# Kernel tuning notes

Measured on AMD Instinct MI355X. Metric: run time of the kernel, lower is better.

The kernel has to match this reference:

```python
import jax, jax.numpy as jnp
import numpy as np

N, E, D_IN, D_OUT = 50000, 800000, 96, 256
BN_EPS = 1e-3  # Keras BatchNormalization default epsilon


def setup_inputs() -> dict:
    key = jax.random.key(0)
    ks = jax.random.split(key, 8)
    return {
        "x": jax.random.normal(ks[0], (N, D_IN), dtype=jnp.float32),
        "adj_src": jax.random.randint(ks[1], (E,), 0, N, dtype=jnp.int32),
        "adj_dst": jax.random.randint(ks[2], (E,), 0, N, dtype=jnp.int32),
        "adj_vals": jax.random.uniform(ks[3], (E,), dtype=jnp.float32),
        "eps": jax.random.normal(ks[4], (1,), dtype=jnp.float32) * 0.05,
        "W0": jax.random.normal(ks[5], (D_IN, D_OUT), dtype=jnp.float32) * 0.05,
        "W1": jax.random.normal(ks[6], (D_OUT, D_OUT), dtype=jnp.float32) * 0.05,
        "gamma": jnp.ones((D_OUT,), dtype=jnp.float32),
        "beta": jnp.zeros((D_OUT,), dtype=jnp.float32),
        "bn_mean": jnp.zeros((D_OUT,), dtype=jnp.float32),
        "bn_var": jnp.ones((D_OUT,), dtype=jnp.float32),
    }


def reference(x, adj_src, adj_dst, adj_vals, eps, W0, W1, gamma, beta, bn_mean, bn_var):
    n = x.shape[0]
    # Sparse adjacency SpMM: out[d] = sum_{e: dst(e)=d} vals[e] * x[src(e)]
    msgs = adj_vals[:, None] * x[adj_src]              # [E, D_IN]
    agg = jax.ops.segment_sum(msgs, adj_dst, num_segments=n)  # [N, D_IN]
    h = agg + eps * x                                   # eps residual (GIN)
    # MLP layer 0: matmul -> BN (inference) -> ReLU (dropout identity at eval)
    h = h @ W0                                           # [N, D_OUT]
    h = (h - bn_mean) * jax.lax.rsqrt(bn_var + BN_EPS) * gamma + beta
    h = jax.nn.relu(h)
    # Final matmul
    return h @ W1                                        # [N, D_OUT]
```

## Files before the change

### kernel.cpp

```cpp
#include <hip/hip_runtime.h>

#define D_IN   96
#define D_OUT  256
#define BN_EPS 1e-3f
#define TROWS  32
#define CAP    64
#define N_PAD  50048
#define RS1    104
#define RS2    264

typedef __attribute__((ext_vector_type(8))) short  short8;
typedef __attribute__((ext_vector_type(4))) float  floatx4;

__device__ __forceinline__ unsigned short f2bf(float f) {
    unsigned int u = __float_as_uint(f);
    unsigned int r = u + 0x7FFFu + ((u >> 16) & 1u);
    return (unsigned short)(r >> 16);
}
__device__ __forceinline__ float bfbits(unsigned short u) {
    return __uint_as_float(((unsigned int)u) << 16);
}

template<bool BF16X>
__device__ __forceinline__ void load12(const float* __restrict__ x,
                                       const unsigned short* __restrict__ xbf,
                                       int rowid, int cg, float* o)
{
    if (BF16X) {
        const unsigned short* r = xbf + (size_t)rowid * D_IN + cg * 12;
        ushort4 a = *(const ushort4*)(r);
        ushort4 b = *(const ushort4*)(r + 4);
        ushort4 c = *(const ushort4*)(r + 8);
        o[0] = bfbits(a.x); o[1] = bfbits(a.y); o[2]  = bfbits(a.z); o[3]  = bfbits(a.w);
        o[4] = bfbits(b.x); o[5] = bfbits(b.y); o[6]  = bfbits(b.z); o[7]  = bfbits(b.w);
        o[8] = bfbits(c.x); o[9] = bfbits(c.y); o[10] = bfbits(c.z); o[11] = bfbits(c.w);
    } else {
        const float* r = x + (size_t)rowid * D_IN + cg * 12;
        float4 A = *(const float4*)(r);
        float4 B = *(const float4*)(r + 4);
        float4 C = *(const float4*)(r + 8);
        o[0] = A.x; o[1] = A.y; o[2]  = A.z; o[3]  = A.w;
        o[4] = B.x; o[5] = B.y; o[6]  = B.z; o[7]  = B.w;
        o[8] = C.x; o[9] = C.y; o[10] = C.z; o[11] = C.w;
    }
}

__global__ __launch_bounds__(256) void prep(
    const int* __restrict__ src, const int* __restrict__ dst,
    const float* __restrict__ vals, const float* __restrict__ x,
    const float* __restrict__ W0, const float* __restrict__ W1,
    int* __restrict__ cursor, int* __restrict__ bucket,
    unsigned short* __restrict__ xbf,
    unsigned short* __restrict__ W0p, unsigned short* __restrict__ W1p,
    int E4, int n, int nscat, int nxc)
{
    const int b = blockIdx.x, tid = threadIdx.x;
    if (b < nscat) {
        int t = b * 256 + tid;
        if (t < E4) {
            int4   d4 = ((const int4*)dst)[t];
            int4   s4 = ((const int4*)src)[t];
            float4 v4 = ((const float4*)vals)[t];
#define PUT(dd, ss, vv)                                                    \
            {  unsigned int u = __float_as_uint(vv);                       \
               unsigned int vhi = (u + 0x7FFFu + ((u >> 16) & 1u)) & 0xFFFF0000u; \
               int pos = atomicAdd(&cursor[dd], 1);                        \
               if (pos < CAP) bucket[((dd) << 6) + pos] = (int)(vhi | (unsigned int)(ss)); }
            PUT(d4.x, s4.x, v4.x)
            PUT(d4.y, s4.y, v4.y)
            PUT(d4.z, s4.z, v4.z)
            PUT(d4.w, s4.w, v4.w)
#undef PUT
        }
    } else if (b < nscat + nxc) {
        int t = (b - nscat) * 256 + tid;
        if (t * 4 < n * D_IN) {
            float4 v = *(const float4*)(x + (size_t)t * 4);
            ushort4 o;
            o.x = f2bf(v.x); o.y = f2bf(v.y); o.z = f2bf(v.z); o.w = f2bf(v.w);
            *(ushort4*)(xbf + (size_t)t * 4) = o;
        }
    } else {
        int o = (b - nscat - nxc) * 256 + tid;
        const int n0 = 3 * 256 * 32;
        const int n1 = 8 * 256 * 32;
        if (o < n0) {
            int kk = o & 31, nn = (o >> 5) & 255, kb = o >> 13;
            W0p[o] = f2bf(W0[(size_t)(kb * 32 + kk) * 256 + nn]);
        } else if (o < n0 + n1) {
            int o2 = o - n0;
            int kk = o2 & 31, nn = (o2 >> 5) & 255, kb = o2 >> 13;
            W1p[o2] = f2bf(W1[(size_t)(kb * 32 + kk) * 256 + nn]);
        }
    }
}

template<bool BF16X>
__global__ __launch_bounds__(256) void gin_fused(
    const float* __restrict__ x, const unsigned short* __restrict__ xbf,
    const int* __restrict__ deg, const int* __restrict__ bucket,
    const float* __restrict__ epsp,
    const unsigned short* __restrict__ W0p, const unsigned short* __restrict__ W1p,
    const float* __restrict__ gamma, const float* __restrict__ beta,
    const float* __restrict__ bn_mean, const float* __restrict__ bn_var,
    float* __restrict__ out, int n)
{
    __shared__ __align__(16) unsigned short Abuf[TROWS][RS1];
    __shared__ __align__(16) unsigned short Hbuf[TROWS][RS2];
    __shared__ float bn_scale[D_OUT];
    __shared__ float bn_shift[D_OUT];

    const int tid = threadIdx.x;
    const int rowbase = blockIdx.x * TROWS;
    const float epsv = *epsp;

    {
        float sc = gamma[tid] * rsqrtf(bn_var[tid] + BN_EPS);
        bn_scale[tid] = sc;
        bn_shift[tid] = fmaf(-bn_mean[tid], sc, beta[tid]);
    }

    {
        const int w  = tid >> 6;
        const int es = (tid & 63) >> 3;
        const int cg = tid & 7;

        for (int rr = 0; rr < 8; ++rr) {
            const int rl  = w * 8 + rr;
            const int row = rowbase + rl;
            float accp[12];
#pragma unroll
            for (int q = 0; q < 12; ++q) accp[q] = 0.f;

            if (row < n) {
                const int dg = min(deg[row], CAP);
                const int* ep = bucket + (row << 6);
                int e = es;
                for (; e + 8 < dg; e += 16) {
                    int p0 = ep[e], p1 = ep[e + 8];
                    float r0[12], r1[12];
                    load12<BF16X>(x, xbf, p0 & 0xFFFF, cg, r0);
                    load12<BF16X>(x, xbf, p1 & 0xFFFF, cg, r1);
                    float v0 = __uint_as_float((unsigned int)p0 & 0xFFFF0000u);
                    float v1 = __uint_as_float((unsigned int)p1 & 0xFFFF0000u);
#pragma unroll
                    for (int q = 0; q < 12; ++q) {
                        accp[q] = fmaf(v0, r0[q], accp[q]);
                        accp[q] = fmaf(v1, r1[q], accp[q]);
                    }
                }
                if (e < dg) {
                    int p0 = ep[e];
                    float r0[12];
                    load12<BF16X>(x, xbf, p0 & 0xFFFF, cg, r0);
                    float v0 = __uint_as_float((unsigned int)p0 & 0xFFFF0000u);
#pragma unroll
                    for (int q = 0; q < 12; ++q)
                        accp[q] = fmaf(v0, r0[q], accp[q]);
                }
            }

#pragma unroll
            for (int q = 0; q < 12; ++q) {
                accp[q] += __shfl_xor(accp[q], 8, 64);
                accp[q] += __shfl_xor(accp[q], 16, 64);
                accp[q] += __shfl_xor(accp[q], 32, 64);
            }

            if (es == 0) {
                if (row < n) {
                    float rx[12];
                    load12<BF16X>(x, xbf, row, cg, rx);
#pragma unroll
                    for (int q = 0; q < 12; ++q)
                        accp[q] = fmaf(epsv, rx[q], accp[q]);
                }
#pragma unroll
                for (int q = 0; q < 6; ++q) {
                    unsigned int lo = f2bf(accp[2 * q]);
                    unsigned int hi = f2bf(accp[2 * q + 1]);
                    *(unsigned int*)&Abuf[rl][cg * 12 + 2 * q] = lo | (hi << 16);
                }
            }
        }
    }
    __syncthreads();

    const int lane = tid & 63;
    const int wid  = tid >> 6;
    const int quad = lane >> 4;
    const int nl   = lane & 15;

    floatx4 acc1[2][4];
#pragma unroll
    for (int mt = 0; mt < 2; ++mt)
#pragma unroll
        for (int nt = 0; nt < 4; ++nt)
            acc1[mt][nt] = (floatx4){0.f, 0.f, 0.f, 0.f};

#pragma unroll
    for (int kb = 0; kb < 3; ++kb) {
        short8 af0 = *(const short8*)&Abuf[nl     ][kb * 32 + quad * 8];
        short8 af1 = *(const short8*)&Abuf[16 + nl][kb * 32 + quad * 8];
#pragma unroll
        for (int nt = 0; nt < 4; ++nt) {
            const unsigned short* bp =
                W0p + ((size_t)(kb * 256 + wid * 64 + nt * 16 + nl)) * 32 + quad * 8;
            short8 bf = *(const short8*)bp;
            acc1[0][nt] = __builtin_amdgcn_mfma_f32_16x16x32_bf16(af0, bf, acc1[0][nt], 0, 0, 0);
            acc1[1][nt] = __builtin_amdgcn_mfma_f32_16x16x32_bf16(af1, bf, acc1[1][nt], 0, 0, 0);
        }
    }

#pragma unroll
    for (int mt = 0; mt < 2; ++mt)
#pragma unroll
        for (int nt = 0; nt < 4; ++nt) {
            int ncol = wid * 64 + nt * 16 + nl;
            float sc = bn_scale[ncol], sh = bn_shift[ncol];
#pragma unroll
            for (int r = 0; r < 4; ++r) {
                float h = fmaxf(0.f, fmaf(acc1[mt][nt][r], sc, sh));
                Hbuf[mt * 16 + quad * 4 + r][ncol] = f2bf(h);
            }
        }
    __syncthreads();

    floatx4 acc2[2][4];
#pragma unroll
    for (int mt = 0; mt < 2; ++mt)
#pragma unroll
        for (int nt = 0; nt < 4; ++nt)
            acc2[mt][nt] = (floatx4){0.f, 0.f, 0.f, 0.f};

#pragma unroll
    for (int kb = 0; kb < 8; ++kb) {
        short8 af0 = *(const short8*)&Hbuf[nl     ][kb * 32 + quad * 8];
        short8 af1 = *(const short8*)&Hbuf[16 + nl][kb * 32 + quad * 8];
#pragma unroll
        for (int nt = 0; nt < 4; ++nt) {
            const unsigned short* bp =
                W1p + ((size_t)(kb * 256 + wid * 64 + nt * 16 + nl)) * 32 + quad * 8;
            short8 bf = *(const short8*)bp;
            acc2[0][nt] = __builtin_amdgcn_mfma_f32_16x16x32_bf16(af0, bf, acc2[0][nt], 0, 0, 0);
            acc2[1][nt] = __builtin_amdgcn_mfma_f32_16x16x32_bf16(af1, bf, acc2[1][nt], 0, 0, 0);
        }
    }

#pragma unroll
    for (int mt = 0; mt < 2; ++mt)
#pragma unroll
        for (int nt = 0; nt < 4; ++nt) {
            int ncol = wid * 64 + nt * 16 + nl;
#pragma unroll
            for (int r = 0; r < 4; ++r) {
                int m = rowbase + mt * 16 + quad * 4 + r;
                if (m < n) out[(size_t)m * D_OUT + ncol] = acc2[mt][nt][r];
            }
        }
}

extern "C" void kernel_launch(void* const* d_in, const int* in_sizes, int n_in,
                              void* d_out, int out_size, void* d_ws, size_t ws_size,
                              hipStream_t stream) {
    const float* x       = (const float*)d_in[0];
    const int*   src     = (const int*)  d_in[1];
    const int*   dst     = (const int*)  d_in[2];
    const float* vals    = (const float*)d_in[3];
    const float* epsp    = (const float*)d_in[4];
    const float* W0      = (const float*)d_in[5];
    const float* W1      = (const float*)d_in[6];
    const float* gamma   = (const float*)d_in[7];
    const float* beta    = (const float*)d_in[8];
    const float* bn_mean = (const float*)d_in[9];
    const float* bn_var  = (const float*)d_in[10];
    float* out = (float*)d_out;

    const int n = in_sizes[0] / D_IN;
    const int E = in_sizes[1];

    int* cursor = (int*)d_ws;
    int* bucket = cursor + N_PAD;
    unsigned short* W0p = (unsigned short*)(bucket + (size_t)n * CAP);
    unsigned short* W1p = W0p + 3 * 256 * 32;
    unsigned short* xbf = W1p + 8 * 256 * 32;

    const size_t base_need = (size_t)(N_PAD + (size_t)n * CAP) * 4
                           + (size_t)(3 + 8) * 256 * 32 * 2;
    const bool use_bf16x = ws_size >= base_need + (size_t)n * D_IN * 2;

    hipMemsetAsync(cursor, 0, (size_t)n * sizeof(int), stream);

    const int E4    = E / 4;
    const int nscat = (E4 + 255) / 256;
    const int nxc   = use_bf16x ? (n * D_IN / 4 + 255) / 256 : 0;
    const int nwc   = ((3 + 8) * 256 * 32 + 255) / 256;
    prep<<<nscat + nxc + nwc, 256, 0, stream>>>(
        src, dst, vals, x, W0, W1, cursor, bucket, xbf, W0p, W1p, E4, n, nscat, nxc);

    const int gblocks = (n + TROWS - 1) / TROWS;
    if (use_bf16x)
        gin_fused<true><<<gblocks, 256, 0, stream>>>(
            x, xbf, cursor, bucket, epsp, W0p, W1p,
            gamma, beta, bn_mean, bn_var, out, n);
    else
        gin_fused<false><<<gblocks, 256, 0, stream>>>(
            x, xbf, cursor, bucket, epsp, W0p, W1p,
            gamma, beta, bn_mean, bn_var, out, n);
}
```

Baseline: 229.4 us.

## Make each wave own 16 rows end-to-end and split atomic cursors by edge parity

The fused kernel is restructured so that each wavefront processes its own 16 rows through gather, both MFMA matmuls and the store, which removes the block-wide __syncthreads barriers. In the gather, 4 lanes now cover one row with 24 features each, replacing the 8-way edge split and its shuffle reduction. The scatter builds two sub-buckets per destination, keyed by edge parity, to halve contention on each atomic counter. BN scale and shift are precomputed once in the prep kernel. The trade-off is that every wave now reads all of W0 and W1 on its own, the per-lane register footprint grows, and each sub-bucket is capped at 32 edges.

```diff
diff --git a/kernel.cpp b/kernel.cpp
--- a/kernel.cpp
+++ b/kernel.cpp
@@ -1,16 +1,17 @@
 #include <hip/hip_runtime.h>
 
-#define D_IN   96
-#define D_OUT  256
-#define BN_EPS 1e-3f
-#define TROWS  32
-#define CAP    64
-#define N_PAD  50048
-#define RS1    104
-#define RS2    264
-
-typedef __attribute__((ext_vector_type(8))) short  short8;
-typedef __attribute__((ext_vector_type(4))) float  floatx4;
+#define D_IN    96
+#define D_OUT   256
+#define BN_EPS  1e-3f
+#define CAP     64
+#define SUBCAP  32
+#define N_PAD   50048
+#define RS1     104
+#define RS2     264
+
+typedef __attribute__((ext_vector_type(8))) short          short8;
+typedef __attribute__((ext_vector_type(8))) unsigned short ushort8;
+typedef __attribute__((ext_vector_type(4))) float          floatx4;
 
 __device__ __forceinline__ unsigned short f2bf(float f) {
     unsigned int u = __float_as_uint(f);
@@ -22,26 +23,26 @@
 }
 
 template<bool BF16X>
-__device__ __forceinline__ void load12(const float* __restrict__ x,
+__device__ __forceinline__ void load24(const float* __restrict__ x,
                                        const unsigned short* __restrict__ xbf,
-                                       int rowid, int cg, float* o)
+                                       int rowid, int j, float* o)
 {
     if (BF16X) {
-        const unsigned short* r = xbf + (size_t)rowid * D_IN + cg * 12;
-        ushort4 a = *(const ushort4*)(r);
-        ushort4 b = *(const ushort4*)(r + 4);
-        ushort4 c = *(const ushort4*)(r + 8);
-        o[0] = bfbits(a.x); o[1] = bfbits(a.y); o[2]  = bfbits(a.z); o[3]  = bfbits(a.w);
-        o[4] = bfbits(b.x); o[5] = bfbits(b.y); o[6]  = bfbits(b.z); o[7]  = bfbits(b.w);
-        o[8] = bfbits(c.x); o[9] = bfbits(c.y); o[10] = bfbits(c.z); o[11] = bfbits(c.w);
+        const ushort8* p = (const ushort8*)(xbf + (size_t)rowid * D_IN + j * 24);
+        ushort8 a = p[0], b = p[1], c = p[2];
+#pragma unroll
+        for (int q = 0; q < 8; ++q) {
+            o[q]      = bfbits(a[q]);
+            o[8 + q]  = bfbits(b[q]);
+            o[16 + q] = bfbits(c[q]);
+        }
     } else {
-        const float* r = x + (size_t)rowid * D_IN + cg * 12;
-        float4 A = *(const float4*)(r);
-        float4 B = *(const float4*)(r + 4);
-        float4 C = *(const float4*)(r + 8);
-        o[0] = A.x; o[1] = A.y; o[2]  = A.z; o[3]  = A.w;
-        o[4] = B.x; o[5] = B.y; o[6]  = B.z; o[7]  = B.w;
-        o[8] = C.x; o[9] = C.y; o[10] = C.z; o[11] = C.w;
+        const float4* p = (const float4*)(x + (size_t)rowid * D_IN + j * 24);
+#pragma unroll
+        for (int q = 0; q < 6; ++q) {
+            float4 v = p[q];
+            o[4 * q] = v.x; o[4 * q + 1] = v.y; o[4 * q + 2] = v.z; o[4 * q + 3] = v.w;
+        }
     }
 }
 
@@ -49,28 +50,25 @@
     const int* __restrict__ src, const int* __restrict__ dst,
     const float* __restrict__ vals, const float* __restrict__ x,
     const float* __restrict__ W0, const float* __restrict__ W1,
+    const float* __restrict__ gamma, const float* __restrict__ beta,
+    const float* __restrict__ bn_mean, const float* __restrict__ bn_var,
     int* __restrict__ cursor, int* __restrict__ bucket,
     unsigned short* __restrict__ xbf,
     unsigned short* __restrict__ W0p, unsigned short* __restrict__ W1p,
-    int E4, int n, int nscat, int nxc)
+    float* __restrict__ bnsc, float* __restrict__ bnsh,
+    int E, int n, int nscat, int nxc)
 {
     const int b = blockIdx.x, tid = threadIdx.x;
     if (b < nscat) {
         int t = b * 256 + tid;
-        if (t < E4) {
-            int4   d4 = ((const int4*)dst)[t];
-            int4   s4 = ((const int4*)src)[t];
-            float4 v4 = ((const float4*)vals)[t];
-#define PUT(dd, ss, vv)                                                    \
-            {  unsigned int u = __float_as_uint(vv);                       \
-               unsigned int vhi = (u + 0x7FFFu + ((u >> 16) & 1u)) & 0xFFFF0000u; \
-               int pos = atomicAdd(&cursor[dd], 1);                        \
-               if (pos < CAP) bucket[((dd) << 6) + pos] = (int)(vhi | (unsigned int)(ss)); }
-            PUT(d4.x, s4.x, v4.x)
-            PUT(d4.y, s4.y, v4.y)
-            PUT(d4.z, s4.z, v4.z)
-            PUT(d4.w, s4.w, v4.w)
-#undef PUT
+        if (t < E) {
+            int d = dst[t];
+            unsigned int u = __float_as_uint(vals[t]);
+            unsigned int vhi = (u + 0x7FFFu + ((u >> 16) & 1u)) & 0xFFFF0000u;
+            int par = t & 1;
+            int pos = atomicAdd(&cursor[2 * d + par], 1);
+            if (pos < SUBCAP)
+                bucket[(d << 6) + par * SUBCAP + pos] = (int)(vhi | (unsigned int)src[t]);
         }
     } else if (b < nscat + nxc) {
         int t = (b - nscat) * 256 + tid;
@@ -91,6 +89,11 @@
             int o2 = o - n0;
             int kk = o2 & 31, nn = (o2 >> 5) & 255, kb = o2 >> 13;
             W1p[o2] = f2bf(W1[(size_t)(kb * 32 + kk) * 256 + nn]);
+        } else if (o < n0 + n1 + D_OUT) {
+            int col = o - n0 - n1;
+            float sc = gamma[col] * rsqrtf(bn_var[col] + BN_EPS);
+            bnsc[col] = sc;
+            bnsh[col] = fmaf(-bn_mean[col], sc, beta[col]);
         }
     }
 }
@@ -98,166 +101,135 @@
 template<bool BF16X>
 __global__ __launch_bounds__(256) void gin_fused(
     const float* __restrict__ x, const unsigned short* __restrict__ xbf,
-    const int* __restrict__ deg, const int* __restrict__ bucket,
+    const int* __restrict__ cursor, const int* __restrict__ bucket,
     const float* __restrict__ epsp,
     const unsigned short* __restrict__ W0p, const unsigned short* __restrict__ W1p,
-    const float* __restrict__ gamma, const float* __restrict__ beta,
-    const float* __restrict__ bn_mean, const float* __restrict__ bn_var,
+    const float* __restrict__ bnsc, const float* __restrict__ bnsh,
     float* __restrict__ out, int n)
 {
-    __shared__ __align__(16) unsigned short Abuf[TROWS][RS1];
-    __shared__ __align__(16) unsigned short Hbuf[TROWS][RS2];
-    __shared__ float bn_scale[D_OUT];
-    __shared__ float bn_shift[D_OUT];
-
-    const int tid = threadIdx.x;
-    const int rowbase = blockIdx.x * TROWS;
+    __shared__ __align__(16) unsigned short Abuf[4][16][RS1];
+    __shared__ __align__(16) unsigned short Hbuf[4][16][RS2];
+
+    const int tid  = threadIdx.x;
+    const int wv   = tid >> 6;
+    const int lane = tid & 63;
+    const int rowbase = blockIdx.x * 64 + wv * 16;
     const float epsv = *epsp;
 
     {
-        float sc = gamma[tid] * rsqrtf(bn_var[tid] + BN_EPS);
-        bn_scale[tid] = sc;
-        bn_shift[tid] = fmaf(-bn_mean[tid], sc, beta[tid]);
-    }
-
-    {
-        const int w  = tid >> 6;
-        const int es = (tid & 63) >> 3;
-        const int cg = tid & 7;
-
-        for (int rr = 0; rr < 8; ++rr) {
-            const int rl  = w * 8 + rr;
-            const int row = rowbase + rl;
-            float accp[12];
-#pragma unroll
-            for (int q = 0; q < 12; ++q) accp[q] = 0.f;
-
-            if (row < n) {
-                const int dg = min(deg[row], CAP);
-                const int* ep = bucket + (row << 6);
-                int e = es;
-                for (; e + 8 < dg; e += 16) {
-                    int p0 = ep[e], p1 = ep[e + 8];
-                    float r0[12], r1[12];
-                    load12<BF16X>(x, xbf, p0 & 0xFFFF, cg, r0);
-                    load12<BF16X>(x, xbf, p1 & 0xFFFF, cg, r1);
-                    float v0 = __uint_as_float((unsigned int)p0 & 0xFFFF0000u);
-                    float v1 = __uint_as_float((unsigned int)p1 & 0xFFFF0000u);
-#pragma unroll
-                    for (int q = 0; q < 12; ++q) {
-                        accp[q] = fmaf(v0, r0[q], accp[q]);
-                        accp[q] = fmaf(v1, r1[q], accp[q]);
-                    }
-                }
-                if (e < dg) {
-                    int p0 = ep[e];
-                    float r0[12];
-                    load12<BF16X>(x, xbf, p0 & 0xFFFF, cg, r0);
-                    float v0 = __uint_as_float((unsigned int)p0 & 0xFFFF0000u);
-#pragma unroll
-                    for (int q = 0; q < 12; ++q)
-                        accp[q] = fmaf(v0, r0[q], accp[q]);
+        const int rl = lane >> 2;
+        const int j  = lane & 3;
+        const int row = rowbase + rl;
+        float accp[24];
+#pragma unroll
+        for (int q = 0; q < 24; ++q) accp[q] = 0.f;
+
+        if (row < n) {
+            const int d0 = min(cursor[2 * row], SUBCAP);
+            const int d1 = min(cursor[2 * row + 1], SUBCAP);
+            const int cnt = d0 + d1;
+            const int* ep = bucket + ((size_t)row << 6);
+            int i = 0;
+            for (; i + 2 <= cnt; i += 2) {
+                int i0 = (i     < d0) ? i     : i     - d0 + SUBCAP;
+                int i1 = (i + 1 < d0) ? i + 1 : i + 1 - d0 + SUBCAP;
+                int p0 = ep[i0], p1 = ep[i1];
+                float r0[24], r1[24];
+                load24<BF16X>(x, xbf, p0 & 0xFFFF, j, r0);
+                load24<BF16X>(x, xbf, p1 & 0xFFFF, j, r1);
+                float v0 = __uint_as_float((unsigned int)p0 & 0xFFFF0000u);
+                float v1 = __uint_as_float((unsigned int)p1 & 0xFFFF0000u);
+#pragma unroll
+                for (int q = 0; q < 24; ++q) {
+                    accp[q] = fmaf(v0, r0[q], accp[q]);
+                    accp[q] = fmaf(v1, r1[q], accp[q]);
                 }
             }
-
-#pragma unroll
-            for (int q = 0; q < 12; ++q) {
-                accp[q] += __shfl_xor(accp[q], 8, 64);
-                accp[q] += __shfl_xor(accp[q], 16, 64);
-                accp[q] += __shfl_xor(accp[q], 32, 64);
+            if (i < cnt) {
+                int i0 = (i < d0) ? i : i - d0 + SUBCAP;
+                int p0 = ep[i0];
+                float r0[24];
+                load24<BF16X>(x, xbf, p0 & 0xFFFF, j, r0);
+                float v0 = __uint_as_float((unsigned int)p0 & 0xFFFF0000u);
+#pragma unroll
+                for (int q = 0; q < 24; ++q)
+                    accp[q] = fmaf(v0, r0[q], accp[q]);
             }
-
-            if (es == 0) {
-                if (row < n) {
-                    float rx[12];
-                    load12<BF16X>(x, xbf, row, cg, rx);
-#pragma unroll
-                    for (int q = 0; q < 12; ++q)
-                        accp[q] = fmaf(epsv, rx[q], accp[q]);
-                }
-#pragma unroll
-                for (int q = 0; q < 6; ++q) {
-                    unsigned int lo = f2bf(accp[2 * q]);
-                    unsigned int hi = f2bf(accp[2 * q + 1]);
-                    *(unsigned int*)&Abuf[rl][cg * 12 + 2 * q] = lo | (hi << 16);
-                }
-            }
-        }
-    }
-    __syncthreads();
-
-    const int lane = tid & 63;
-    const int wid  = tid >> 6;
+            float rx[24];
+            load24<BF16X>(x, xbf, row, j, rx);
+#pragma unroll
+            for (int q = 0; q < 24; ++q)
+                accp[q] = fmaf(epsv, rx[q], accp[q]);
+        }
+#pragma unroll
+        for (int g = 0; g < 3; ++g) {
+            short8 s;
+#pragma unroll
+            for (int q = 0; q < 8; ++q)
+                s[q] = (short)f2bf(accp[g * 8 + q]);
+            *(short8*)&Abuf[wv][rl][j * 24 + g * 8] = s;
+        }
+    }
+
     const int quad = lane >> 4;
     const int nl   = lane & 15;
 
-    floatx4 acc1[2][4];
-#pragma unroll
-    for (int mt = 0; mt < 2; ++mt)
-#pragma unroll
-        for (int nt = 0; nt < 4; ++nt)
-            acc1[mt][nt] = (floatx4){0.f, 0.f, 0.f, 0.f};
+    short8 af[3];
+#pragma unroll
+    for (int kb = 0; kb < 3; ++kb)
+        af[kb] = *(const short8*)&Abuf[wv][nl][kb * 32 + quad * 8];
+
+    floatx4 acc1[16];
+#pragma unroll
+    for (int nt = 0; nt < 16; ++nt)
+        acc1[nt] = (floatx4){0.f, 0.f, 0.f, 0.f};
 
 #pragma unroll
     for (int kb = 0; kb < 3; ++kb) {
-        short8 af0 = *(const short8*)&Abuf[nl     ][kb * 32 + quad * 8];
-        short8 af1 = *(const short8*)&Abuf[16 + nl][kb * 32 + quad * 8];
-#pragma unroll
-        for (int nt = 0; nt < 4; ++nt) {
-            const unsigned short* bp =
-                W0p + ((size_t)(kb * 256 + wid * 64 + nt * 16 + nl)) * 32 + quad * 8;
-            short8 bf = *(const short8*)bp;
-            acc1[0][nt] = __builtin_amdgcn_mfma_f32_16x16x32_bf16(af0, bf, acc1[0][nt], 0, 0, 0);
-            acc1[1][nt] = __builtin_amdgcn_mfma_f32_16x16x32_bf16(af1, bf, acc1[1][nt], 0, 0, 0);
-        }
-    }
-
-#pragma unroll
-    for (int mt = 0; mt < 2; ++mt)
-#pragma unroll
-        for (int nt = 0; nt < 4; ++nt) {
-            int ncol = wid * 64 + nt * 16 + nl;
-            float sc = bn_scale[ncol], sh = bn_shift[ncol];
-#pragma unroll
-            for (int r = 0; r < 4; ++r) {
-                float h = fmaxf(0.f, fmaf(acc1[mt][nt][r], sc, sh));
-                Hbuf[mt * 16 + quad * 4 + r][ncol] = f2bf(h);
-            }
-        }
-    __syncthreads();
-
-    floatx4 acc2[2][4];
-#pragma unroll
-    for (int mt = 0; mt < 2; ++mt)
-#pragma unroll
-        for (int nt = 0; nt < 4; ++nt)
-            acc2[mt][nt] = (floatx4){0.f, 0.f, 0.f, 0.f};
+#pragma unroll
+        for (int nt = 0; nt < 16; ++nt) {
+            const short8 bf = *(const short8*)(
+                W0p + ((size_t)(kb * 256 + nt * 16 + nl)) * 32 + quad * 8);
+            acc1[nt] = __builtin_amdgcn_mfma_f32_16x16x32_bf16(af[kb], bf, acc1[nt], 0, 0, 0);
+        }
+    }
+
+#pragma unroll
+    for (int nt = 0; nt < 16; ++nt) {
+        const int ncol = nt * 16 + nl;
+        const float sc = bnsc[ncol], sh = bnsh[ncol];
+#pragma unroll
+        for (int r = 0; r < 4; ++r) {
+            float h = fmaxf(0.f, fmaf(acc1[nt][r], sc, sh));
+            Hbuf[wv][quad * 4 + r][ncol] = f2bf(h);
+        }
+    }
+
+    floatx4 acc2[16];
+#pragma unroll
+    for (int nt = 0; nt < 16; ++nt)
+        acc2[nt] = (floatx4){0.f, 0.f, 0.f, 0.f};
 
 #pragma unroll
     for (int kb = 0; kb < 8; ++kb) {
-        short8 af0 = *(const short8*)&Hbuf[nl     ][kb * 32 + quad * 8];
-        short8 af1 = *(const short8*)&Hbuf[16 + nl][kb * 32 + quad * 8];
-#pragma unroll
-        for (int nt = 0; nt < 4; ++nt) {
-            const unsigned short* bp =
-                W1p + ((size_t)(kb * 256 + wid * 64 + nt * 16 + nl)) * 32 + quad * 8;
-            short8 bf = *(const short8*)bp;
-            acc2[0][nt] = __builtin_amdgcn_mfma_f32_16x16x32_bf16(af0, bf, acc2[0][nt], 0, 0, 0);
-            acc2[1][nt] = __builtin_amdgcn_mfma_f32_16x16x32_bf16(af1, bf, acc2[1][nt], 0, 0, 0);
-        }
-    }
-
-#pragma unroll
-    for (int mt = 0; mt < 2; ++mt)
-#pragma unroll
-        for (int nt = 0; nt < 4; ++nt) {
-            int ncol = wid * 64 + nt * 16 + nl;
-#pragma unroll
-            for (int r = 0; r < 4; ++r) {
-                int m = rowbase + mt * 16 + quad * 4 + r;
-                if (m < n) out[(size_t)m * D_OUT + ncol] = acc2[mt][nt][r];
-            }
-        }
+        const short8 af2 = *(const short8*)&Hbuf[wv][nl][kb * 32 + quad * 8];
+#pragma unroll
+        for (int nt = 0; nt < 16; ++nt) {
+            const short8 bf = *(const short8*)(
+                W1p + ((size_t)(kb * 256 + nt * 16 + nl)) * 32 + quad * 8);
+            acc2[nt] = __builtin_amdgcn_mfma_f32_16x16x32_bf16(af2, bf, acc2[nt], 0, 0, 0);
+        }
+    }
+
+#pragma unroll
+    for (int nt = 0; nt < 16; ++nt) {
+        const int ncol = nt * 16 + nl;
+#pragma unroll
+        for (int r = 0; r < 4; ++r) {
+            int m = rowbase + quad * 4 + r;
+            if (m < n) out[(size_t)m * D_OUT + ncol] = acc2[nt][r];
+        }
+    }
 }
 
 extern "C" void kernel_launch(void* const* d_in, const int* in_sizes, int n_in,
@@ -280,31 +252,31 @@
     const int E = in_sizes[1];
 
     int* cursor = (int*)d_ws;
-    int* bucket = cursor + N_PAD;
-    unsigned short* W0p = (unsigned short*)(bucket + (size_t)n * CAP);
+    int* bucket = cursor + 2 * N_PAD;
+    float* bnsc = (float*)(bucket + (size_t)n * CAP);
+    float* bnsh = bnsc + D_OUT;
+    unsigned short* W0p = (unsigned short*)(bnsh + D_OUT);
     unsigned short* W1p = W0p + 3 * 256 * 32;
     unsigned short* xbf = W1p + 8 * 256 * 32;
 
-    const size_t base_need = (size_t)(N_PAD + (size_t)n * CAP) * 4
+    const size_t base_need = ((size_t)2 * N_PAD + (size_t)n * CAP + 2 * D_OUT) * 4
                            + (size_t)(3 + 8) * 256 * 32 * 2;
     const bool use_bf16x = ws_size >= base_need + (size_t)n * D_IN * 2;
 
-    hipMemsetAsync(cursor, 0, (size_t)n * sizeof(int), stream);
-
-    const int E4    = E / 4;
-    const int nscat = (E4 + 255) / 256;
+    hipMemsetAsync(cursor, 0, (size_t)2 * n * sizeof(int), stream);
+
+    const int nscat = (E + 255) / 256;
     const int nxc   = use_bf16x ? (n * D_IN / 4 + 255) / 256 : 0;
-    const int nwc   = ((3 + 8) * 256 * 32 + 255) / 256;
+    const int nwc   = ((3 + 8) * 256 * 32 + D_OUT + 255) / 256;
     prep<<<nscat + nxc + nwc, 256, 0, stream>>>(
-        src, dst, vals, x, W0, W1, cursor, bucket, xbf, W0p, W1p, E4, n, nscat, nxc);
-
-    const int gblocks = (n + TROWS - 1) / TROWS;
+        src, dst, vals, x, W0, W1, gamma, beta, bn_mean, bn_var,
+        cursor, bucket, xbf, W0p, W1p, bnsc, bnsh, E, n, nscat, nxc);
+
+    const int gblocks = (n + 63) / 64;
     if (use_bf16x)
         gin_fused<true><<<gblocks, 256, 0, stream>>>(
-            x, xbf, cursor, bucket, epsp, W0p, W1p,
-            gamma, beta, bn_mean, bn_var, out, n);
+            x, xbf, cursor, bucket, epsp, W0p, W1p, bnsc, bnsh, out, n);
     else
         gin_fused<false><<<gblocks, 256, 0, stream>>>(
-            x, xbf, cursor, bucket, epsp, W0p, W1p,
-            gamma, beta, bn_mean, bn_var, out, n);
-}
+            x, xbf, cursor, bucket, epsp, W0p, W1p, bnsc, bnsh, out, n);
+}
```

New measurement: 213.8 us. -6.8%, faster.
